# Kernel optimization log

Measured on AMD Instinct MI355X. Metric: run time of the kernel, lower is better.

## Reference

```python
import jax, jax.numpy as jnp
import numpy as np

R, N, H, T, E = 8, 100000, 128, 64, 50000


def setup_inputs() -> dict:
    key = jax.random.key(0)
    ks = jax.random.split(key, 12)
    s = 1.0 / np.sqrt(H)
    inp = {
        # learned params
        "prev_embeddings": jax.random.normal(ks[0], (R, N, H), jnp.float32),
        "enc_W": jax.random.normal(ks[1], (2 * R, H, T), jnp.float32) * (1.0 / np.sqrt(T)),
        "enc_b": jax.random.normal(ks[2], (2 * R, H), jnp.float32) * 0.01,
        "W_ih": jax.random.normal(ks[3], (R, 3 * H, 2 * H), jnp.float32) * s,
        "W_hh": jax.random.normal(ks[4], (R, 3 * H, H), jnp.float32) * s,
        "b_ih": jax.random.normal(ks[5], (R, 3 * H), jnp.float32) * s,
        "b_hh": jax.random.normal(ks[6], (R, 3 * H), jnp.float32) * s,
        # edge list
        "src": jax.random.randint(ks[7], (E,), 0, N, jnp.int32),
        "dst": jax.random.randint(ks[8], (E,), 0, N, jnp.int32),
        "rel": jax.random.randint(ks[9], (E,), 0, R, jnp.int32),
        "t_edge": jax.random.randint(ks[10], (E,), 0, 100, jnp.int32),
        "current_time": 100,
    }
    return inp


def reference(prev_embeddings, enc_W, enc_b, W_ih, W_hh, b_ih, b_hh, src, dst, rel, t_edge, current_time):
    Rr, Nn, Hh = prev_embeddings.shape
    Tt = enc_W.shape[-1]
    Ee = src.shape[0]

    # time one-hot -> Linear == column gather of encoder weight + bias (rel>=0 path)
    bucket = jnp.minimum(current_time - t_edge, Tt - 1)          # [E]
    encoded = enc_W[rel, :, bucket] + enc_b[rel]                 # [E,H]

    u_i = prev_embeddings[rel, src]                              # [E,H] (also h_prev)
    u_j = prev_embeddings[rel, dst]                              # [E,H]
    x = jnp.concatenate([encoded + u_j, u_i], axis=-1)           # [E,2H]
    h_prev = u_i

    # per-relation GRUCell, vectorized over edges; select by relation id
    h_new = jnp.zeros_like(h_prev)
    for r in range(Rr):
        gi = x @ W_ih[r].T + b_ih[r]                             # [E,3H]
        gh = h_prev @ W_hh[r].T + b_hh[r]                        # [E,3H]
        i_r, i_z, i_n = jnp.split(gi, 3, axis=-1)
        h_r, h_z, h_n = jnp.split(gh, 3, axis=-1)
        rg = jax.nn.sigmoid(i_r + h_r)
        zg = jax.nn.sigmoid(i_z + h_z)
        ng = jnp.tanh(i_n + rg * h_n)
        cand = (1.0 - zg) * ng + zg * h_prev
        h_new = jnp.where((rel == r)[:, None], cand, h_new)

    arangeE = jnp.arange(Ee, dtype=jnp.int32)
    flat_key = rel * Nn + src
    last_pos = jnp.full(Rr * Nn, -1, jnp.int32).at[flat_key].max(arangeE)
    is_last = arangeE == last_pos[flat_key]
    tgt = jnp.where(is_last, src, Nn)                            # route dups to pad row

    updated = jnp.concatenate(
        [prev_embeddings, jnp.zeros((Rr, 1, Hh), prev_embeddings.dtype)], axis=1)
    updated = updated.at[rel, tgt].set(h_new)
    return updated[:, :Nn]
```

## Files before the change

kernel.cpp:

```cpp
#include <hip/hip_runtime.h>
#include <math.h>

#define HH   128
#define HH2  256
#define HH3  384
#define MB   16
#define TBK  512


__global__ void k_lastpos(const int* __restrict__ rel, const int* __restrict__ src,
                          int* __restrict__ lastpos, int N, int E) {
  int e = blockIdx.x * 256 + threadIdx.x;
  if (e >= E) return;
  atomicMax(&lastpos[rel[e] * N + src[e]], e);
}

__global__ void k_count(const int* __restrict__ rel, const int* __restrict__ src,
                        const int* __restrict__ lastpos, int* __restrict__ meta,
                        int N, int E) {
  int e = blockIdx.x * 256 + threadIdx.x;
  if (e >= E) return;
  int r = rel[e];
  if (lastpos[r * N + src[e]] == e) atomicAdd(&meta[r], 1);
}

__global__ void k_scan(int* __restrict__ meta, int R) {
  if (threadIdx.x != 0 || blockIdx.x != 0) return;
  int off = 0, g = 0;
  meta[16] = 0; meta[33] = 0;
  for (int r = 0; r < R; r++) {
    int c = meta[r];
    off += c;
    g += (c + MB - 1) / MB;
    meta[16 + r + 1] = off;
    meta[33 + r + 1] = g;
    meta[51 + r] = meta[16 + r];
  }
  meta[50] = g;
}

__global__ void k_scatter(const int* __restrict__ rel, const int* __restrict__ src,
                          const int* __restrict__ lastpos, int* __restrict__ meta,
                          int* __restrict__ bin, int N, int E) {
  int e = blockIdx.x * 256 + threadIdx.x;
  if (e >= E) return;
  int r = rel[e];
  if (lastpos[r * N + src[e]] == e) {
    int p = atomicAdd(&meta[51 + r], 1);
    bin[p] = e;
  }
}

__global__ void k_transpose(const float* __restrict__ W, float* __restrict__ Wt,
                            int rows, int cols, int total) {
  int idx = blockIdx.x * 256 + threadIdx.x;
  if (idx >= total) return;
  int per = rows * cols;
  int r = idx / per;
  int rem = idx - r * per;
  int c = rem / rows;
  int row = rem - c * rows;
  Wt[idx] = W[(size_t)r * per + (size_t)row * cols + c];
}

__global__ void k_et(const float* __restrict__ encW, const float* __restrict__ encB,
                     float* __restrict__ ET, int R, int T) {
  int idx = blockIdx.x * 256 + threadIdx.x;
  int total = R * TBK * HH;
  if (idx >= total) return;
  int r = idx / (TBK * HH);
  int rem = idx - r * (TBK * HH);
  int b = rem / HH;
  int h = rem - b * HH;
  float v = 0.0f;
  if (b < T) v = encW[((size_t)r * HH + h) * (size_t)T + b] + encB[r * HH + h];
  ET[idx] = v;
}

__global__ void k_copy(const float4* __restrict__ in, float4* __restrict__ o, long long n4) {
  long long i = (long long)blockIdx.x * blockDim.x + threadIdx.x;
  long long stride = (long long)gridDim.x * blockDim.x;
  for (; i < n4; i += stride) o[i] = in[i];
}

__global__ __launch_bounds__(128) void k_gru(
    const float* __restrict__ prev, const float* __restrict__ encW, const float* __restrict__ encB,
    const float* __restrict__ bih, const float* __restrict__ bhh,
    const int* __restrict__ src, const int* __restrict__ dst, const int* __restrict__ te,
    const int* __restrict__ ctp,
    const int* __restrict__ meta, const int* __restrict__ bin,
    const float* __restrict__ WtIh, const float* __restrict__ WtHh, const float* __restrict__ ET,
    float* __restrict__ out, int N, int T, int R) {
  int b = blockIdx.x;
  int total = meta[50];
  if (b >= total) return;
  int r = 0;
  while (r + 1 < R && b >= meta[33 + r + 1]) r++;
  int g = b - meta[33 + r];
  int i0 = meta[16 + r] + g * MB;
  int mcnt = meta[16 + r + 1] - i0;
  if (mcnt > MB) mcnt = MB;

  __shared__ float xs[MB][HH2];
  __shared__ int sS[MB], sD[MB], sB[MB];
  int h = threadIdx.x;

  if (h < MB) {
    if (h < mcnt) {
      int e = bin[i0 + h];
      sS[h] = src[e];
      sD[h] = dst[e];
      int bk = *ctp - te[e];
      if (bk > T - 1) bk = T - 1;
      sB[h] = bk;
    } else {
      sS[h] = 0; sD[h] = 0; sB[h] = 0;
    }
  }
  __syncthreads();

  #pragma unroll
  for (int m = 0; m < MB; m++) {
    if (m < mcnt) {
      int s = sS[m], d = sD[m], bk = sB[m];
      float ui = prev[((size_t)r * N + s) * HH + h];
      float uj = prev[((size_t)r * N + d) * HH + h];
      float enc;
      if (bk < TBK) enc = ET[((size_t)r * TBK + bk) * HH + h];
      else          enc = encW[((size_t)r * HH + h) * (size_t)T + bk] + encB[r * HH + h];
      xs[m][h]      = enc + uj;
      xs[m][HH + h] = ui;
    } else {
      xs[m][h] = 0.0f; xs[m][HH + h] = 0.0f;
    }
  }
  __syncthreads();

  float a_r[MB], a_z[MB], a_in[MB], a_hn[MB];
  #pragma unroll
  for (int m = 0; m < MB; m++) { a_r[m] = 0.f; a_z[m] = 0.f; a_in[m] = 0.f; a_hn[m] = 0.f; }

  const float* Wi = WtIh + (size_t)r * HH2 * HH3;
  for (int j = 0; j < HH2; j += 4) {
    float wr[4], wz[4], wn[4];
    #pragma unroll
    for (int u = 0; u < 4; u++) {
      const float* row = Wi + (size_t)(j + u) * HH3;
      wr[u] = row[h]; wz[u] = row[HH + h]; wn[u] = row[2 * HH + h];
    }
    #pragma unroll
    for (int m = 0; m < MB; m++) {
      float4 xv = *(const float4*)&xs[m][j];
      a_r[m]  += xv.x * wr[0] + xv.y * wr[1] + xv.z * wr[2] + xv.w * wr[3];
      a_z[m]  += xv.x * wz[0] + xv.y * wz[1] + xv.z * wz[2] + xv.w * wz[3];
      a_in[m] += xv.x * wn[0] + xv.y * wn[1] + xv.z * wn[2] + xv.w * wn[3];
    }
  }

  const float* Wh = WtHh + (size_t)r * HH * HH3;
  for (int j = 0; j < HH; j += 4) {
    float wr[4], wz[4], wn[4];
    #pragma unroll
    for (int u = 0; u < 4; u++) {
      const float* row = Wh + (size_t)(j + u) * HH3;
      wr[u] = row[h]; wz[u] = row[HH + h]; wn[u] = row[2 * HH + h];
    }
    #pragma unroll
    for (int m = 0; m < MB; m++) {
      float4 xv = *(const float4*)&xs[m][HH + j];
      a_r[m]  += xv.x * wr[0] + xv.y * wr[1] + xv.z * wr[2] + xv.w * wr[3];
      a_z[m]  += xv.x * wz[0] + xv.y * wz[1] + xv.z * wz[2] + xv.w * wz[3];
      a_hn[m] += xv.x * wn[0] + xv.y * wn[1] + xv.z * wn[2] + xv.w * wn[3];
    }
  }

  float bir = bih[r * HH3 + h], biz = bih[r * HH3 + HH + h], bin2 = bih[r * HH3 + 2 * HH + h];
  float bhr = bhh[r * HH3 + h], bhz = bhh[r * HH3 + HH + h], bhn  = bhh[r * HH3 + 2 * HH + h];

  for (int m = 0; m < mcnt; m++) {
    float rg = 1.f / (1.f + __expf(-(a_r[m] + bir + bhr)));
    float zg = 1.f / (1.f + __expf(-(a_z[m] + biz + bhz)));
    float ng = tanhf(a_in[m] + bin2 + rg * (a_hn[m] + bhn));
    float hp = xs[m][HH + h];
    out[((size_t)r * N + sS[m]) * HH + h] = (1.f - zg) * ng + zg * hp;
  }
}


extern "C" void kernel_launch(void* const* d_in, const int* in_sizes, int n_in,
                              void* d_out, int out_size, void* d_ws, size_t ws_size,
                              hipStream_t stream) {
  const float* prev = (const float*)d_in[0];
  const float* encW = (const float*)d_in[1];
  const float* encB = (const float*)d_in[2];
  const float* Wih  = (const float*)d_in[3];
  const float* Whh  = (const float*)d_in[4];
  const float* bih  = (const float*)d_in[5];
  const float* bhh  = (const float*)d_in[6];
  const int* src = (const int*)d_in[7];
  const int* dst = (const int*)d_in[8];
  const int* rel = (const int*)d_in[9];
  const int* te  = (const int*)d_in[10];
  const int* ctp = (const int*)d_in[11];
  float* out = (float*)d_out;

  int E = in_sizes[7];
  int R = in_sizes[5] / HH3;
  int N = in_sizes[0] / (R * HH);
  int T = in_sizes[1] / (2 * R * HH);

  int* lastpos = (int*)d_ws;
  int* meta = lastpos + (size_t)R * N;
  int* bin = meta + 128;
  size_t off = (size_t)R * N + 128 + E;
  off = (off + 3) & ~(size_t)3;
  float* WtIh = (float*)d_ws + off;  off += (size_t)R * HH2 * HH3;
  float* WtHh = (float*)d_ws + off;  off += (size_t)R * HH * HH3;
  float* ET   = (float*)d_ws + off;  off += (size_t)R * TBK * HH;
  (void)ws_size;

  hipMemsetAsync(lastpos, 0xFF, (size_t)R * N * sizeof(int), stream);
  hipMemsetAsync(meta, 0, 128 * sizeof(int), stream);

  int eb = (E + 255) / 256;
  k_lastpos<<<eb, 256, 0, stream>>>(rel, src, lastpos, N, E);
  k_count<<<eb, 256, 0, stream>>>(rel, src, lastpos, meta, N, E);
  k_scan<<<1, 64, 0, stream>>>(meta, R);
  k_scatter<<<eb, 256, 0, stream>>>(rel, src, lastpos, meta, bin, N, E);

  int tIh = R * HH3 * HH2;
  int tHh = R * HH3 * HH;
  k_transpose<<<(tIh + 255) / 256, 256, 0, stream>>>(Wih, WtIh, HH3, HH2, tIh);
  k_transpose<<<(tHh + 255) / 256, 256, 0, stream>>>(Whh, WtHh, HH3, HH, tHh);
  int tET = R * TBK * HH;
  k_et<<<(tET + 255) / 256, 256, 0, stream>>>(encW, encB, ET, R, T);

  long long n4 = (long long)out_size / 4;
  k_copy<<<8192, 256, 0, stream>>>((const float4*)prev, (float4*)out, n4);

  int gruBlocks = (E + MB - 1) / MB + R;
  k_gru<<<gruBlocks, 128, 0, stream>>>(prev, encW, encB, bih, bhh, src, dst, te, ctp,
                                       meta, bin, WtIh, WtHh, ET, out, N, T, R);
}
```

Measured before the change: 1.360 ms.

## Move GRU gate GEMM to bf16 MFMA with split hi/lo precision

```diff
diff --git a/kernel.cpp b/kernel.cpp
--- a/kernel.cpp
+++ b/kernel.cpp
@@ -2,10 +2,20 @@
 #include <math.h>
 
 #define HH   128
-#define HH2  256
-#define HH3  384
-#define MB   16
+#define KK   256
+#define NC   512
+#define MB   32
 #define TBK  512
+
+typedef short bf16x8 __attribute__((ext_vector_type(8)));
+typedef float f32x4  __attribute__((ext_vector_type(4)));
+
+__device__ __forceinline__ float bf2f(short s) {
+  union { unsigned u; float f; } v; v.u = ((unsigned)(unsigned short)s) << 16; return v.f;
+}
+__device__ __forceinline__ short f2bf(float f) {
+  union { float f; unsigned u; } v; v.f = f; return (short)(v.u >> 16);
+}
 
 
 __global__ void k_lastpos(const int* __restrict__ rel, const int* __restrict__ src,
@@ -51,16 +61,28 @@
   }
 }
 
-__global__ void k_transpose(const float* __restrict__ W, float* __restrict__ Wt,
-                            int rows, int cols, int total) {
+__global__ void k_wprep(const float* __restrict__ Wih, const float* __restrict__ Whh,
+                        short* __restrict__ WThi, short* __restrict__ WTlo, int R) {
   int idx = blockIdx.x * 256 + threadIdx.x;
+  int total = R * NC * KK;
   if (idx >= total) return;
-  int per = rows * cols;
-  int r = idx / per;
-  int rem = idx - r * per;
-  int c = rem / rows;
-  int row = rem - c * rows;
-  Wt[idx] = W[(size_t)r * per + (size_t)row * cols + c];
+  int r = idx / (NC * KK);
+  int rem = idx - r * (NC * KK);
+  int c = rem >> 8;
+  int j = rem & 255;
+  float w = 0.0f;
+  if (c < 256) {
+    w = Wih[((size_t)r * 384 + c) * 256 + j];
+    if (j >= 128) w += Whh[((size_t)r * 384 + c) * 128 + (j - 128)];
+  } else if (c < 384) {
+    w = Wih[((size_t)r * 384 + c) * 256 + j];
+  } else {
+    if (j >= 128) w = Whh[((size_t)r * 384 + (c - 128)) * 128 + (j - 128)];
+  }
+  short hi = f2bf(w);
+  short lo = f2bf(w - bf2f(hi));
+  WThi[idx] = hi;
+  WTlo[idx] = lo;
 }
 
 __global__ void k_et(const float* __restrict__ encW, const float* __restrict__ encB,
@@ -83,15 +105,20 @@
   for (; i < n4; i += stride) o[i] = in[i];
 }
 
-__global__ __launch_bounds__(128) void k_gru(
+__global__ __launch_bounds__(256, 2) void k_gru(
     const float* __restrict__ prev, const float* __restrict__ encW, const float* __restrict__ encB,
     const float* __restrict__ bih, const float* __restrict__ bhh,
     const int* __restrict__ src, const int* __restrict__ dst, const int* __restrict__ te,
     const int* __restrict__ ctp,
     const int* __restrict__ meta, const int* __restrict__ bin,
-    const float* __restrict__ WtIh, const float* __restrict__ WtHh, const float* __restrict__ ET,
+    const short* __restrict__ WThi, const short* __restrict__ WTlo, const float* __restrict__ ET,
     float* __restrict__ out, int N, int T, int R) {
-  int b = blockIdx.x;
+  int nwg = gridDim.x;
+  int orig = blockIdx.x;
+  int q = nwg >> 3, rm = nwg & 7;
+  int xcd = orig & 7, oi = orig >> 3;
+  int b = (xcd < rm ? xcd * (q + 1) : rm * (q + 1) + (xcd - rm) * q) + oi;
+
   int total = meta[50];
   if (b >= total) return;
   int r = 0;
@@ -101,88 +128,115 @@
   int mcnt = meta[16 + r + 1] - i0;
   if (mcnt > MB) mcnt = MB;
 
-  __shared__ float xs[MB][HH2];
-  __shared__ int sS[MB], sD[MB], sB[MB];
-  int h = threadIdx.x;
-
-  if (h < MB) {
-    if (h < mcnt) {
-      int e = bin[i0 + h];
-      sS[h] = src[e];
-      sD[h] = dst[e];
+  __shared__ __align__(16) short Ahi[MB * KK];
+  __shared__ __align__(16) short Alo[MB * KK];
+  __shared__ int sS[MB], sB[MB], sD[MB];
+
+  int t = threadIdx.x;
+  if (t < MB) {
+    if (t < mcnt) {
+      int e = bin[i0 + t];
+      sS[t] = src[e];
+      sD[t] = dst[e];
       int bk = *ctp - te[e];
       if (bk > T - 1) bk = T - 1;
-      sB[h] = bk;
+      sB[t] = bk;
     } else {
-      sS[h] = 0; sD[h] = 0; sB[h] = 0;
+      sS[t] = 0; sD[t] = 0; sB[t] = 0;
     }
   }
   __syncthreads();
 
+  #pragma unroll 4
+  for (int m = 0; m < MB; m++) {
+    int s = sS[m], d = sD[m], bk = sB[m];
+    float v;
+    if (t < HH) {
+      float enc;
+      if (bk < TBK) enc = ET[((size_t)r * TBK + bk) * HH + t];
+      else          enc = encW[((size_t)r * HH + t) * (size_t)T + bk] + encB[r * HH + t];
+      v = enc + prev[((size_t)r * N + d) * HH + t];
+    } else {
+      v = prev[((size_t)r * N + s) * HH + (t - HH)];
+    }
+    short hi = f2bf(v);
+    short lo = f2bf(v - bf2f(hi));
+    int idx = (m * KK + t) ^ ((m & 7) << 3);
+    Ahi[idx] = hi;
+    Alo[idx] = lo;
+  }
+  __syncthreads();
+
+  int lane = t & 63;
+  int w = t >> 6;
+  int lm = lane & 15;
+  int lg = lane >> 4;
+
+  f32x4 acc[4][2][2];
   #pragma unroll
-  for (int m = 0; m < MB; m++) {
-    if (m < mcnt) {
-      int s = sS[m], d = sD[m], bk = sB[m];
-      float ui = prev[((size_t)r * N + s) * HH + h];
-      float uj = prev[((size_t)r * N + d) * HH + h];
-      float enc;
-      if (bk < TBK) enc = ET[((size_t)r * TBK + bk) * HH + h];
-      else          enc = encW[((size_t)r * HH + h) * (size_t)T + bk] + encB[r * HH + h];
-      xs[m][h]      = enc + uj;
-      xs[m][HH + h] = ui;
-    } else {
-      xs[m][h] = 0.0f; xs[m][HH + h] = 0.0f;
-    }
-  }
-  __syncthreads();
-
-  float a_r[MB], a_z[MB], a_in[MB], a_hn[MB];
+  for (int a = 0; a < 4; a++)
+    #pragma unroll
+    for (int mf = 0; mf < 2; mf++)
+      #pragma unroll
+      for (int cf = 0; cf < 2; cf++)
+        acc[a][mf][cf] = (f32x4){0.f, 0.f, 0.f, 0.f};
+
+  const short* WH = WThi + (size_t)r * NC * KK;
+  const short* WL = WTlo + (size_t)r * NC * KK;
+
+  for (int ks = 0; ks < 8; ks++) {
+    bf16x8 ah[2], al[2];
+    #pragma unroll
+    for (int mf = 0; mf < 2; mf++) {
+      int m = mf * 16 + lm;
+      int idx = (m * KK + ks * 32 + lg * 8) ^ ((m & 7) << 3);
+      ah[mf] = *(const bf16x8*)&Ahi[idx];
+      al[mf] = *(const bf16x8*)&Alo[idx];
+    }
+    #pragma unroll
+    for (int cf = 0; cf < 2; cf++) {
+      #pragma unroll
+      for (int gate = 0; gate < 4; gate++) {
+        int c = gate * HH + w * 32 + cf * 16 + lm;
+        size_t off = (size_t)c * KK + ks * 32 + lg * 8;
+        bf16x8 bh = *(const bf16x8*)&WH[off];
+        bf16x8 bl = *(const bf16x8*)&WL[off];
+        #pragma unroll
+        for (int mf = 0; mf < 2; mf++) {
+          acc[gate][mf][cf] = __builtin_amdgcn_mfma_f32_16x16x32_bf16(ah[mf], bh, acc[gate][mf][cf], 0, 0, 0);
+          acc[gate][mf][cf] = __builtin_amdgcn_mfma_f32_16x16x32_bf16(al[mf], bh, acc[gate][mf][cf], 0, 0, 0);
+          acc[gate][mf][cf] = __builtin_amdgcn_mfma_f32_16x16x32_bf16(ah[mf], bl, acc[gate][mf][cf], 0, 0, 0);
+        }
+      }
+    }
+  }
+
   #pragma unroll
-  for (int m = 0; m < MB; m++) { a_r[m] = 0.f; a_z[m] = 0.f; a_in[m] = 0.f; a_hn[m] = 0.f; }
-
-  const float* Wi = WtIh + (size_t)r * HH2 * HH3;
-  for (int j = 0; j < HH2; j += 4) {
-    float wr[4], wz[4], wn[4];
-    #pragma unroll
-    for (int u = 0; u < 4; u++) {
-      const float* row = Wi + (size_t)(j + u) * HH3;
-      wr[u] = row[h]; wz[u] = row[HH + h]; wn[u] = row[2 * HH + h];
-    }
-    #pragma unroll
-    for (int m = 0; m < MB; m++) {
-      float4 xv = *(const float4*)&xs[m][j];
-      a_r[m]  += xv.x * wr[0] + xv.y * wr[1] + xv.z * wr[2] + xv.w * wr[3];
-      a_z[m]  += xv.x * wz[0] + xv.y * wz[1] + xv.z * wz[2] + xv.w * wz[3];
-      a_in[m] += xv.x * wn[0] + xv.y * wn[1] + xv.z * wn[2] + xv.w * wn[3];
-    }
-  }
-
-  const float* Wh = WtHh + (size_t)r * HH * HH3;
-  for (int j = 0; j < HH; j += 4) {
-    float wr[4], wz[4], wn[4];
-    #pragma unroll
-    for (int u = 0; u < 4; u++) {
-      const float* row = Wh + (size_t)(j + u) * HH3;
-      wr[u] = row[h]; wz[u] = row[HH + h]; wn[u] = row[2 * HH + h];
-    }
-    #pragma unroll
-    for (int m = 0; m < MB; m++) {
-      float4 xv = *(const float4*)&xs[m][HH + j];
-      a_r[m]  += xv.x * wr[0] + xv.y * wr[1] + xv.z * wr[2] + xv.w * wr[3];
-      a_z[m]  += xv.x * wz[0] + xv.y * wz[1] + xv.z * wz[2] + xv.w * wz[3];
-      a_hn[m] += xv.x * wn[0] + xv.y * wn[1] + xv.z * wn[2] + xv.w * wn[3];
-    }
-  }
-
-  float bir = bih[r * HH3 + h], biz = bih[r * HH3 + HH + h], bin2 = bih[r * HH3 + 2 * HH + h];
-  float bhr = bhh[r * HH3 + h], bhz = bhh[r * HH3 + HH + h], bhn  = bhh[r * HH3 + 2 * HH + h];
-
-  for (int m = 0; m < mcnt; m++) {
-    float rg = 1.f / (1.f + __expf(-(a_r[m] + bir + bhr)));
-    float zg = 1.f / (1.f + __expf(-(a_z[m] + biz + bhz)));
-    float ng = tanhf(a_in[m] + bin2 + rg * (a_hn[m] + bhn));
-    float hp = xs[m][HH + h];
-    out[((size_t)r * N + sS[m]) * HH + h] = (1.f - zg) * ng + zg * hp;
+  for (int cf = 0; cf < 2; cf++) {
+    int c = w * 32 + cf * 16 + lm;
+    float bR = bih[r * 384 + c]       + bhh[r * 384 + c];
+    float bZ = bih[r * 384 + HH + c]  + bhh[r * 384 + HH + c];
+    float bN = bih[r * 384 + 2 * HH + c];
+    float bH = bhh[r * 384 + 2 * HH + c];
+    #pragma unroll
+    for (int mf = 0; mf < 2; mf++) {
+      #pragma unroll
+      for (int reg = 0; reg < 4; reg++) {
+        int m = mf * 16 + lg * 4 + reg;
+        if (m < mcnt) {
+          float sr  = acc[0][mf][cf][reg] + bR;
+          float sz  = acc[1][mf][cf][reg] + bZ;
+          float in_ = acc[2][mf][cf][reg] + bN;
+          float hn  = acc[3][mf][cf][reg] + bH;
+          float rg = 1.f / (1.f + __expf(-sr));
+          float zg = 1.f / (1.f + __expf(-sz));
+          float ng = tanhf(in_ + rg * hn);
+          int idxh = (m * KK + HH + c) ^ ((m & 7) << 3);
+          float hp = bf2f(Ahi[idxh]) + bf2f(Alo[idxh]);
+          out[((size_t)r * N + sS[m]) * HH + c] = (1.f - zg) * ng + zg * hp;
+        }
+      }
+    }
   }
 }
 
@@ -205,18 +259,19 @@
   float* out = (float*)d_out;
 
   int E = in_sizes[7];
-  int R = in_sizes[5] / HH3;
+  int R = in_sizes[5] / 384;
   int N = in_sizes[0] / (R * HH);
   int T = in_sizes[1] / (2 * R * HH);
 
-  int* lastpos = (int*)d_ws;
-  int* meta = lastpos + (size_t)R * N;
-  int* bin = meta + 128;
-  size_t off = (size_t)R * N + 128 + E;
-  off = (off + 3) & ~(size_t)3;
-  float* WtIh = (float*)d_ws + off;  off += (size_t)R * HH2 * HH3;
-  float* WtHh = (float*)d_ws + off;  off += (size_t)R * HH * HH3;
-  float* ET   = (float*)d_ws + off;  off += (size_t)R * TBK * HH;
+  char* wsb = (char*)d_ws;
+  size_t off = 0;
+  int* lastpos = (int*)(wsb + off); off += (size_t)R * N * 4;
+  int* meta    = (int*)(wsb + off); off += 128 * 4;
+  int* bin     = (int*)(wsb + off); off += (size_t)E * 4;
+  off = (off + 15) & ~(size_t)15;
+  short* WThi = (short*)(wsb + off); off += (size_t)R * NC * KK * 2;
+  short* WTlo = (short*)(wsb + off); off += (size_t)R * NC * KK * 2;
+  float* ET   = (float*)(wsb + off); off += (size_t)R * TBK * HH * 4;
   (void)ws_size;
 
   hipMemsetAsync(lastpos, 0xFF, (size_t)R * N * sizeof(int), stream);
@@ -228,10 +283,8 @@
   k_scan<<<1, 64, 0, stream>>>(meta, R);
   k_scatter<<<eb, 256, 0, stream>>>(rel, src, lastpos, meta, bin, N, E);
 
-  int tIh = R * HH3 * HH2;
-  int tHh = R * HH3 * HH;
-  k_transpose<<<(tIh + 255) / 256, 256, 0, stream>>>(Wih, WtIh, HH3, HH2, tIh);
-  k_transpose<<<(tHh + 255) / 256, 256, 0, stream>>>(Whh, WtHh, HH3, HH, tHh);
+  int tW = R * NC * KK;
+  k_wprep<<<(tW + 255) / 256, 256, 0, stream>>>(Wih, Whh, WThi, WTlo, R);
   int tET = R * TBK * HH;
   k_et<<<(tET + 255) / 256, 256, 0, stream>>>(encW, encB, ET, R, T);
 
@@ -239,6 +292,6 @@
   k_copy<<<8192, 256, 0, stream>>>((const float4*)prev, (float4*)out, n4);
 
   int gruBlocks = (E + MB - 1) / MB + R;
-  k_gru<<<gruBlocks, 128, 0, stream>>>(prev, encW, encB, bih, bhh, src, dst, te, ctp,
-                                       meta, bin, WtIh, WtHh, ET, out, N, T, R);
-}
+  k_gru<<<gruBlocks, 256, 0, stream>>>(prev, encW, encB, bih, bhh, src, dst, te, ctp,
+                                       meta, bin, WThi, WTlo, ET, out, N, T, R);
+}
```

Result: faster. 1.238 ms (-9.0%).
